# Optimization experiments

Measured on AMD Instinct MI355X. Metric: run time of the kernel, lower is better.

The kernel has to match this reference:

```python
import jax, jax.numpy as jnp
import numpy as np

EPS = 1e-5

def setup_inputs() -> dict:
    key = jax.random.key(0)
    ks = jax.random.split(key, 6)
    N, E, C, H, L = 50000, 800000, 128, 128, 3
    x = jax.random.normal(ks[0], (N, C), dtype=jnp.float32)
    edge_index = jax.random.randint(ks[1], (2, E), 0, N, dtype=jnp.int64)
    # Xavier-ish scaled weights; layer 0 uses in=C=H so all layers stack uniformly.
    Wl = jax.random.normal(ks[2], (L, C, H), dtype=jnp.float32) / np.sqrt(C)
    Wr = jax.random.normal(ks[3], (L, C, H), dtype=jnp.float32) / np.sqrt(C)
    b = jnp.zeros((L, H), dtype=jnp.float32)
    gamma = jnp.ones((L, H), dtype=jnp.float32)
    beta = jnp.zeros((L, H), dtype=jnp.float32)
    return {"x": x, "edge_index": edge_index, "Wl": Wl, "Wr": Wr, "b": b,
            "gamma": gamma, "beta": beta}

def _sage_bn_relu(x, src, dst, Wl, Wr, b, gamma, beta):
    N = x.shape[0]
    # mean aggregation of source features into target nodes (PyG SAGEConv default)
    agg = jax.ops.segment_sum(x[src], dst, num_segments=N)          # [N, C]
    deg = jax.ops.segment_sum(jnp.ones_like(dst, dtype=x.dtype), dst, num_segments=N)
    mean_nbr = agg / jnp.maximum(deg, 1.0)[:, None]
    h = mean_nbr @ Wl + x @ Wr + b                                   # [N, H]
    # BatchNorm1d (training-mode batch statistics over nodes)
    mu = jnp.mean(h, axis=0)
    var = jnp.var(h, axis=0)
    h = gamma * (h - mu) * jax.lax.rsqrt(var + EPS) + beta
    return jax.nn.relu(h)  # dropout omitted (deterministic reference, p->0)

def reference(x, edge_index, Wl, Wr, b, gamma, beta):
    src, dst = edge_index[0], edge_index[1]
    h = x
    for l in range(Wl.shape[0]):
        h = _sage_bn_relu(h, src, dst, Wl[l], Wr[l], b[l], gamma[l], beta[l])
    return h
```

## Files before the change

kernel.cpp:

```cpp
#include <hip/hip_runtime.h>
#include <hip/hip_bf16.h>

#define BN_EPS 1e-5f
#define NPASS 4
#define NKEY 512
#define BCAP2 6144

typedef unsigned short u16;
typedef unsigned int u32;
typedef __attribute__((ext_vector_type(8))) short bf16x8v;
typedef __attribute__((ext_vector_type(4))) float f32x4v;

__device__ __forceinline__ float bf2f(u16 u){
    union { u32 i; float f; } c; c.i = ((u32)u) << 16; return c.f;
}
__device__ __forceinline__ u16 f2bf(float f){
    union { float f; u32 i; } c; c.f = f;
    u32 x = c.i;
    u32 r = x + 0x7FFFu + ((x >> 16) & 1u);
    return (u16)(r >> 16);
}
__device__ __forceinline__ float lo16(u32 u){
    union { u32 i; float f; } c; c.i = u << 16; return c.f;
}
__device__ __forceinline__ float hi16(u32 u){
    union { u32 i; float f; } c; c.i = u & 0xFFFF0000u; return c.f;
}
__device__ __forceinline__ u32 pack2(float f0, float f1){
    return (u32)f2bf(f0) | ((u32)f2bf(f1) << 16);
}

__global__ void detect_k(const int* __restrict__ ei, const u16* __restrict__ xu,
                         int* __restrict__ flags){
    int lane = threadIdx.x;
    unsigned long long bal = __ballot(ei[2 * lane + 1] != 0);
    int cnt = 0;
    #pragma unroll
    for (int k = 0; k < 4; ++k){
        u16 u = xu[2 * (lane + 64 * k)];
        int e = (u >> 7) & 0xFF;
        cnt += (e >= 0x70 && e <= 0x86) ? 1 : 0;
    }
    #pragma unroll
    for (int off = 1; off < 64; off <<= 1) cnt += __shfl_xor(cnt, off);
    if (lane == 0){
        flags[0] = (bal == 0ULL) ? 1 : 0;
        flags[1] = (cnt >= 128) ? 1 : 0;
    }
}

__global__ void prep_k(const void* __restrict__ x, const void* __restrict__ Wl,
                       const void* __restrict__ Wr, const void* __restrict__ b,
                       const void* __restrict__ g, const void* __restrict__ be,
                       u16* __restrict__ xb, u16* __restrict__ wT, float* __restrict__ p,
                       int total4, int wtot, int per, const int* __restrict__ flags){
    int i = blockIdx.x * blockDim.x + threadIdx.x;
    int bf = flags[1];
    if (i < total4){
        if (bf){
            ((uint2*)xb)[i] = ((const uint2*)x)[i];
        } else {
            float4 v = ((const float4*)x)[i];
            ushort4 o; o.x = f2bf(v.x); o.y = f2bf(v.y); o.z = f2bf(v.z); o.w = f2bf(v.w);
            ((ushort4*)xb)[i] = o;
        }
    }
    if (i < wtot){
        u16 vl = bf ? ((const u16*)Wl)[i] : f2bf(((const float*)Wl)[i]);
        u16 vr = bf ? ((const u16*)Wr)[i] : f2bf(((const float*)Wr)[i]);
        int l = i >> 14, r = (i >> 7) & 127, c = i & 127;
        wT[(size_t)(l * 2 + 0) * 16384 + c * 128 + r] = vl;
        wT[(size_t)(l * 2 + 1) * 16384 + c * 128 + r] = vr;
    }
    if (i < per){
        if (bf){
            p[i]           = bf2f(((const u16*)b)[i]);
            p[per + i]     = bf2f(((const u16*)g)[i]);
            p[2 * per + i] = bf2f(((const u16*)be)[i]);
        } else {
            p[i]           = ((const float*)b)[i];
            p[per + i]     = ((const float*)g)[i];
            p[2 * per + i] = ((const float*)be)[i];
        }
    }
}

__global__ __launch_bounds__(1024) void phist_k(const void* __restrict__ ei, int E,
                                                int tile, u32* __restrict__ blockHist,
                                                const int* __restrict__ flags){
    __shared__ u32 lh[NKEY];
    int tid = threadIdx.x;
    if (tid < NKEY) lh[tid] = 0u;
    __syncthreads();
    int start = blockIdx.x * tile;
    int end = min(E, start + tile);
    int i64 = flags[0];
    for (int i = start + tid; i < end; i += 1024){
        int s, d;
        if (i64){
            const long long* p = (const long long*)ei;
            s = (int)p[i]; d = (int)p[E + i];
        } else {
            const int* p = (const int*)ei;
            s = p[i]; d = p[E + i];
        }
        int key = ((s >> 14) << 7) | (d >> 9);
        atomicAdd(&lh[key], 1u);
    }
    __syncthreads();
    if (tid < NKEY) blockHist[blockIdx.x * NKEY + tid] = lh[tid];
}

__global__ __launch_bounds__(512) void bases_k(const u32* __restrict__ blockHist,
                                               u32* __restrict__ blockBase,
                                               int* __restrict__ rangeBase,
                                               int* __restrict__ rp2N, int nb){
    __shared__ u32 t_s[NKEY];
    int k = threadIdx.x;
    u32 run = 0;
    #pragma unroll 8
    for (int b = 0; b < nb; ++b){
        blockBase[b * NKEY + k] = run;
        run += blockHist[b * NKEY + k];
    }
    t_s[k] = min(run, (u32)BCAP2);
    __syncthreads();
    if (k == 0){
        u32 r = 0;
        for (int j = 0; j < NKEY; ++j){ u32 v = t_s[j]; t_s[j] = r; r += v; }
        rangeBase[NKEY] = (int)r;
        *rp2N = (int)r;
    }
    __syncthreads();
    rangeBase[k] = (int)t_s[k];
}

__global__ __launch_bounds__(1024) void pscat_k(const void* __restrict__ ei, int E,
                                                int tile, const u32* __restrict__ blockBase,
                                                u32* __restrict__ part,
                                                const int* __restrict__ flags){
    __shared__ u32 lcur[NKEY];
    int tid = threadIdx.x;
    if (tid < NKEY) lcur[tid] = blockBase[blockIdx.x * NKEY + tid];
    __syncthreads();
    int start = blockIdx.x * tile;
    int end = min(E, start + tile);
    int i64 = flags[0];
    for (int i = start + tid; i < end; i += 1024){
        int s, d;
        if (i64){
            const long long* p = (const long long*)ei;
            s = (int)p[i]; d = (int)p[E + i];
        } else {
            const int* p = (const int*)ei;
            s = p[i]; d = p[E + i];
        }
        int key = ((s >> 14) << 7) | (d >> 9);
        u32 pos = atomicAdd(&lcur[key], 1u);
        if (pos < BCAP2) part[(size_t)key * BCAP2 + pos] = (u32)(u16)s | ((u32)(d & 511) << 16);
    }
}

__global__ __launch_bounds__(1024) void build_k(const u32* __restrict__ part,
                                                const int* __restrict__ rangeBase,
                                                int* __restrict__ rowptr2,
                                                u16* __restrict__ col, int N){
    __shared__ u32 bins[512];
    __shared__ u32 wsum[8];
    __shared__ u16 sorted[BCAP2];
    int key  = blockIdx.x;
    int tid  = threadIdx.x;
    int base = rangeBase[key];
    int cntk = rangeBase[key + 1] - base;
    int p    = key >> 7;
    int d0   = (key & 127) << 9;
    if (tid < 512) bins[tid] = 0u;
    __syncthreads();
    const u32* pk = part + (size_t)key * BCAP2;
    for (int i = tid; i < cntk; i += 1024)
        atomicAdd(&bins[pk[i] >> 16], 1u);
    __syncthreads();
    int lane = tid & 63, w = tid >> 6;
    u32 v = (tid < 512) ? bins[tid] : 0u;
    u32 sc = v;
    #pragma unroll
    for (int off = 1; off < 64; off <<= 1){
        u32 u = __shfl_up(sc, off);
        if (lane >= off) sc += u;
    }
    if (lane == 63 && w < 8) wsum[w] = sc;
    __syncthreads();
    if (tid == 0){
        u32 r = 0;
        #pragma unroll
        for (int j = 0; j < 8; ++j){ u32 t = wsum[j]; wsum[j] = r; r += t; }
    }
    __syncthreads();
    u32 excl = (w < 8 ? wsum[w] : 0u) + sc - v;
    if (tid < 512){
        int d = d0 + tid;
        if (d < N) rowptr2[(size_t)p * N + d] = base + (int)excl;
        bins[tid] = excl;
    }
    __syncthreads();
    for (int i = tid; i < cntk; i += 1024){
        u32 e = pk[i];
        u32 pos = atomicAdd(&bins[e >> 16], 1u);
        sorted[pos] = (u16)e;
    }
    __syncthreads();
    for (int i = tid; i < cntk; i += 1024)
        col[base + i] = sorted[i];
}

#define ACC8(A, G) \
    A[0] += lo16(G.x); A[1] += hi16(G.x); \
    A[2] += lo16(G.y); A[3] += hi16(G.y); \
    A[4] += lo16(G.z); A[5] += hi16(G.z); \
    A[6] += lo16(G.w); A[7] += hi16(G.w);

__global__ __launch_bounds__(256) void agg_k(const u16* __restrict__ h,
                                             const int* __restrict__ rp2,
                                             const u16* __restrict__ col,
                                             u16* __restrict__ meanb, int N){
    int tid  = threadIdx.x;
    int gwid = (blockIdx.x * 256 + tid) >> 6;
    int lane = tid & 63;
    int quad = lane >> 4;
    int sub  = lane & 15;
    if (gwid * 8 >= N) return;
    int d0 = gwid * 8 + quad * 2;
    int d1 = d0 + 1;

    float a0[8] = {0.f,0.f,0.f,0.f,0.f,0.f,0.f,0.f};
    float a1[8] = {0.f,0.f,0.f,0.f,0.f,0.f,0.f,0.f};
    int g0 = 0, g1 = 0;

    for (int p = 0; p < NPASS; ++p){
        const int* rp = rp2 + (size_t)p * N;
        int s0 = 0, e0 = 0, s1 = 0, e1 = 0;
        if (d0 < N){ s0 = rp[d0]; e0 = rp[d0 + 1]; }
        if (d1 < N){ s1 = rp[d1]; e1 = rp[d1 + 1]; }
        g0 += e0 - s0; g1 += e1 - s1;
        int i0 = s0, i1 = s1;
        for (; i0 + 1 < e0 && i1 + 1 < e1; i0 += 2, i1 += 2){
            int sa = col[i0], sb = col[i0 + 1], sc = col[i1], sd = col[i1 + 1];
            uint4 ga = *(const uint4*)(h + (size_t)sa * 128 + sub * 8);
            uint4 gb = *(const uint4*)(h + (size_t)sb * 128 + sub * 8);
            uint4 gc = *(const uint4*)(h + (size_t)sc * 128 + sub * 8);
            uint4 gd = *(const uint4*)(h + (size_t)sd * 128 + sub * 8);
            ACC8(a0, ga); ACC8(a0, gb);
            ACC8(a1, gc); ACC8(a1, gd);
        }
        for (; i0 + 1 < e0; i0 += 2){
            int sa = col[i0], sb = col[i0 + 1];
            uint4 ga = *(const uint4*)(h + (size_t)sa * 128 + sub * 8);
            uint4 gb = *(const uint4*)(h + (size_t)sb * 128 + sub * 8);
            ACC8(a0, ga); ACC8(a0, gb);
        }
        if (i0 < e0){
            int sa = col[i0];
            uint4 ga = *(const uint4*)(h + (size_t)sa * 128 + sub * 8);
            ACC8(a0, ga);
        }
        for (; i1 + 1 < e1; i1 += 2){
            int sc = col[i1], sd = col[i1 + 1];
            uint4 gc = *(const uint4*)(h + (size_t)sc * 128 + sub * 8);
            uint4 gd = *(const uint4*)(h + (size_t)sd * 128 + sub * 8);
            ACC8(a1, gc); ACC8(a1, gd);
        }
        if (i1 < e1){
            int sc = col[i1];
            uint4 gc = *(const uint4*)(h + (size_t)sc * 128 + sub * 8);
            ACC8(a1, gc);
        }
    }

    if (d0 < N){
        float di = 1.f / fmaxf((float)g0, 1.f);
        uint4 o;
        o.x = pack2(a0[0] * di, a0[1] * di);
        o.y = pack2(a0[2] * di, a0[3] * di);
        o.z = pack2(a0[4] * di, a0[5] * di);
        o.w = pack2(a0[6] * di, a0[7] * di);
        *(uint4*)(meanb + (size_t)d0 * 128 + sub * 8) = o;
    }
    if (d1 < N){
        float di = 1.f / fmaxf((float)g1, 1.f);
        uint4 o;
        o.x = pack2(a1[0] * di, a1[1] * di);
        o.y = pack2(a1[2] * di, a1[3] * di);
        o.z = pack2(a1[4] * di, a1[5] * di);
        o.w = pack2(a1[6] * di, a1[7] * di);
        *(uint4*)(meanb + (size_t)d1 * 128 + sub * 8) = o;
    }
}
#undef ACC8

__global__ __launch_bounds__(256, 2) void gemm_k(
        const u16* __restrict__ Aa, const u16* __restrict__ Ab,
        const u16* __restrict__ wT, const float* __restrict__ bias,
        float* __restrict__ stats, u16* __restrict__ hp16, int N, int NT){
    int tid  = threadIdx.x;
    int lane = tid & 63;
    int w    = tid >> 6;
    int hl   = lane & 15;
    int quad = lane >> 4;
    int c0   = (2 * w)     * 16 + hl;
    int c1   = (2 * w + 1) * 16 + hl;

    bf16x8v Bf[2][2][4];
    {
        const u16* bp = wT + (size_t)(2 * w) * 2048 + (size_t)hl * 128 + quad * 8;
        #pragma unroll
        for (int tl = 0; tl < 2; ++tl)
            #pragma unroll
            for (int half = 0; half < 2; ++half)
                #pragma unroll
                for (int kc = 0; kc < 4; ++kc)
                    Bf[tl][half][kc] =
                        *(const bf16x8v*)(bp + tl * 2048 + half * 16384 + kc * 32);
    }
    float bv0 = bias[c0], bv1 = bias[c1];
    float cs0 = 0.f, cq0 = 0.f, cs1 = 0.f, cq1 = 0.f;

    size_t laneoff = (size_t)hl * 128 + quad * 8;
    bf16x8v AX[2][2][4], AY[2][2][4];

#define LOADA(DST, T) { \
    int m0_ = (T) * 32; \
    int rb0_ = m0_;      if (rb0_ + 16 > N) rb0_ = N - 16; \
    int rb1_ = m0_ + 16; if (rb1_ + 16 > N) rb1_ = N - 16; \
    const u16* pa0_ = Aa + (size_t)rb0_ * 128 + laneoff; \
    const u16* pb0_ = Ab + (size_t)rb0_ * 128 + laneoff; \
    const u16* pa1_ = Aa + (size_t)rb1_ * 128 + laneoff; \
    const u16* pb1_ = Ab + (size_t)rb1_ * 128 + laneoff; \
    _Pragma("unroll") \
    for (int kc_ = 0; kc_ < 4; ++kc_){ \
        DST[0][0][kc_] = *(const bf16x8v*)(pa0_ + kc_ * 32); \
        DST[1][0][kc_] = *(const bf16x8v*)(pa1_ + kc_ * 32); \
        DST[0][1][kc_] = *(const bf16x8v*)(pb0_ + kc_ * 32); \
        DST[1][1][kc_] = *(const bf16x8v*)(pb1_ + kc_ * 32); \
    } }

#define PROC(SRC, T) { \
    int m0_ = (T) * 32; \
    int rb0_ = m0_;      bool v0_ = (m0_ + 16 <= N); if (!v0_) rb0_ = N - 16; \
    int rb1_ = m0_ + 16; bool v1_ = (m0_ + 32 <= N); if (!v1_) rb1_ = N - 16; \
    f32x4v acc0_[2], acc1_[2]; \
    acc0_[0] = (f32x4v){0.f,0.f,0.f,0.f}; acc0_[1] = (f32x4v){0.f,0.f,0.f,0.f}; \
    acc1_[0] = (f32x4v){0.f,0.f,0.f,0.f}; acc1_[1] = (f32x4v){0.f,0.f,0.f,0.f}; \
    _Pragma("unroll") \
    for (int half_ = 0; half_ < 2; ++half_) \
        _Pragma("unroll") \
        for (int kc_ = 0; kc_ < 4; ++kc_) \
            _Pragma("unroll") \
            for (int tl_ = 0; tl_ < 2; ++tl_){ \
                acc0_[tl_] = __builtin_amdgcn_mfma_f32_16x16x32_bf16( \
                    SRC[0][half_][kc_], Bf[tl_][half_][kc_], acc0_[tl_], 0, 0, 0); \
                acc1_[tl_] = __builtin_amdgcn_mfma_f32_16x16x32_bf16( \
                    SRC[1][half_][kc_], Bf[tl_][half_][kc_], acc1_[tl_], 0, 0, 0); \
            } \
    _Pragma("unroll") \
    for (int tl_ = 0; tl_ < 2; ++tl_){ \
        int   c_  = tl_ ? c1 : c0; \
        float bv_ = tl_ ? bv1 : bv0; \
        if (v0_){ \
            _Pragma("unroll") \
            for (int r_ = 0; r_ < 4; ++r_){ \
                float vv_ = acc0_[tl_][r_] + bv_; \
                hp16[(size_t)(rb0_ + quad * 4 + r_) * 128 + c_] = f2bf(vv_); \
                if (tl_){ cs1 += vv_; cq1 += vv_ * vv_; } else { cs0 += vv_; cq0 += vv_ * vv_; } \
            } \
        } \
        if (v1_){ \
            _Pragma("unroll") \
            for (int r_ = 0; r_ < 4; ++r_){ \
                float vv_ = acc1_[tl_][r_] + bv_; \
                hp16[(size_t)(rb1_ + quad * 4 + r_) * 128 + c_] = f2bf(vv_); \
                if (tl_){ cs1 += vv_; cq1 += vv_ * vv_; } else { cs0 += vv_; cq0 += vv_ * vv_; } \
            } \
        } \
    } }

    int t = blockIdx.x;
    int G = gridDim.x;
    if (t < NT){
        LOADA(AX, t);
        for (;;){
            int tn = t + G;
            if (tn < NT) LOADA(AY, tn);
            PROC(AX, t);
            t = tn;
            if (t >= NT) break;
            tn = t + G;
            if (tn < NT) LOADA(AX, tn);
            PROC(AY, t);
            t = tn;
            if (t >= NT) break;
        }
    }
#undef LOADA
#undef PROC

    cs0 += __shfl_xor(cs0, 16); cs0 += __shfl_xor(cs0, 32);
    cq0 += __shfl_xor(cq0, 16); cq0 += __shfl_xor(cq0, 32);
    cs1 += __shfl_xor(cs1, 16); cs1 += __shfl_xor(cs1, 32);
    cq1 += __shfl_xor(cq1, 16); cq1 += __shfl_xor(cq1, 32);
    if (quad == 0){
        float* st = stats + (size_t)(blockIdx.x & 63) * 256;
        atomicAdd(&st[c0],       cs0);
        atomicAdd(&st[128 + c0], cq0);
        atomicAdd(&st[c1],       cs1);
        atomicAdd(&st[128 + c1], cq1);
    }
}

__global__ __launch_bounds__(256) void apply_k(
        const u16* __restrict__ in, const float* __restrict__ stats,
        const float* __restrict__ g, const float* __restrict__ be,
        u16* __restrict__ outb, float* __restrict__ outf, int use_f32,
        int total4, float invN){
    __shared__ float s_red[256];
    __shared__ float s_ss[256];
    int tid = threadIdx.x;
    float s = 0.f;
    #pragma unroll 8
    for (int bkt = 0; bkt < 64; ++bkt) s += stats[bkt * 256 + tid];
    s_red[tid] = s;
    __syncthreads();
    if (tid < 128){
        float mu  = s_red[tid] * invN;
        float var = s_red[128 + tid] * invN - mu * mu;
        if (!(mu == mu)) mu = 0.f;
        if (!(var >= 0.f) || !(var == var)) var = 0.f;
        float sc = g[tid] * rsqrtf(var + BN_EPS);
        s_ss[tid]       = sc;
        s_ss[128 + tid] = be[tid] - mu * sc;
    }
    __syncthreads();
    int c = (tid & 31) * 4;
    float sc0 = s_ss[c],     sh0 = s_ss[128 + c];
    float sc1 = s_ss[c + 1], sh1 = s_ss[129 + c];
    float sc2 = s_ss[c + 2], sh2 = s_ss[130 + c];
    float sc3 = s_ss[c + 3], sh3 = s_ss[131 + c];
    for (int i = blockIdx.x * blockDim.x + tid; i < total4; i += blockDim.x * gridDim.x){
        uint2 u = ((const uint2*)in)[i];
        float4 v;
        v.x = lo16(u.x); v.y = hi16(u.x); v.z = lo16(u.y); v.w = hi16(u.y);
        if (!(v.x == v.x)) v.x = 0.f;
        if (!(v.y == v.y)) v.y = 0.f;
        if (!(v.z == v.z)) v.z = 0.f;
        if (!(v.w == v.w)) v.w = 0.f;
        float r0 = fmaxf(v.x * sc0 + sh0, 0.f);
        float r1 = fmaxf(v.y * sc1 + sh1, 0.f);
        float r2 = fmaxf(v.z * sc2 + sh2, 0.f);
        float r3 = fmaxf(v.w * sc3 + sh3, 0.f);
        if (use_f32){
            float4 o; o.x = r0; o.y = r1; o.z = r2; o.w = r3;
            ((float4*)outf)[i] = o;
        } else {
            uint2 o; o.x = pack2(r0, r1); o.y = pack2(r2, r3);
            ((uint2*)outb)[i] = o;
        }
    }
}

extern "C" void kernel_launch(void* const* d_in, const int* in_sizes, int n_in,
                              void* d_out, int out_size, void* d_ws, size_t ws_size,
                              hipStream_t stream){
    const void* x  = d_in[0];
    const int*  ei = (const int*)d_in[1];
    const void* Wl = d_in[2];
    const void* Wr = d_in[3];
    const void* b  = d_in[4];
    const void* gm = d_in[5];
    const void* bt = d_in[6];
    float* outf = (float*)d_out;

    const int N = in_sizes[0] / 128;
    const int E = in_sizes[1] / 2;
    const int L = in_sizes[2] / 16384;
    const int PB = 128;
    const int TILE = (E + PB - 1) / PB;

    char* wsp = (char*)d_ws;
    size_t off = 0;
    auto alloc = [&](size_t bytes) -> char* {
        char* p = wsp + off;
        off = (off + bytes + 255) & ~(size_t)255;
        return p;
    };
    int*   flags  = (int*)  alloc(16);
    int*   rowptr2= (int*)  alloc(((size_t)NPASS * N + 1) * 4);
    u16*   col    = (u16*)  alloc((size_t)E * 2);
    u32*   bHist  = (u32*)  alloc((size_t)PB * NKEY * 4);
    u32*   bBase  = (u32*)  alloc((size_t)PB * NKEY * 4);
    int*   rangeB = (int*)  alloc((size_t)(NKEY + 1) * 4);
    u32*   part   = (u32*)  alloc((size_t)NKEY * BCAP2 * 4);
    u16*   wT     = (u16*)  alloc((size_t)L * 2 * 16384 * 2);
    float* pvec   = (float*)alloc((size_t)3 * L * 128 * 4);
    float* stats  = (float*)alloc((size_t)L * 64 * 256 * 4);
    u16*   xb     = (u16*)  alloc((size_t)N * 128 * 2);
    u16*   meanb  = (u16*)  alloc((size_t)N * 128 * 2);
    u16*   hpre16 = (u16*)  alloc((size_t)N * 128 * 2);
    u16*   hA     = (u16*)  alloc((size_t)N * 128 * 2);
    u16*   hB     = (u16*)  alloc((size_t)N * 128 * 2);
    (void)ws_size; (void)n_in; (void)out_size;

    detect_k<<<1, 64, 0, stream>>>(ei, (const u16*)x, flags);
    hipMemsetAsync(stats, 0, (size_t)L * 64 * 256 * 4, stream);

    phist_k<<<PB, 1024, 0, stream>>>((const void*)ei, E, TILE, bHist, flags);
    bases_k<<<1, 512, 0, stream>>>(bHist, bBase, rangeB, rowptr2 + (size_t)NPASS * N, PB);
    pscat_k<<<PB, 1024, 0, stream>>>((const void*)ei, E, TILE, bBase, part, flags);
    build_k<<<NKEY, 1024, 0, stream>>>(part, rangeB, rowptr2, col, N);

    prep_k<<<(N * 32 + 255) / 256, 256, 0, stream>>>(x, Wl, Wr, b, gm, bt, xb, wT, pvec,
                                                     N * 32, L * 16384, L * 128, flags);

    const u16* state = xb;
    int NT      = (N + 31) / 32;
    int gblocks = (NT + 2) / 3;
    int nwaves  = (N + 7) / 8;
    int ablocks = (nwaves + 3) / 4;
    float invN  = 1.f / (float)N;
    for (int l = 0; l < L; ++l){
        int last = (l == L - 1);
        u16* nxt = (l & 1) ? hB : hA;
        agg_k<<<ablocks, 256, 0, stream>>>(state, rowptr2, col, meanb, N);
        gemm_k<<<gblocks, 256, 0, stream>>>(meanb, state, wT + (size_t)l * 2 * 16384,
                                            pvec + (size_t)l * 128,
                                            stats + (size_t)l * 64 * 256,
                                            hpre16, N, NT);
        apply_k<<<1024, 256, 0, stream>>>(hpre16, stats + (size_t)l * 64 * 256,
                                          pvec + (size_t)L * 128 + l * 128,
                                          pvec + (size_t)2 * L * 128 + l * 128,
                                          nxt, outf, last, N * 32, invN);
        state = nxt;
    }
}
```

Baseline: 320.1 us.

## Stage GEMM A tiles through swizzled double-buffered LDS shared by all waves

Previously each of the four waves loaded the full 32-row A tile (mean and self features) from global memory into registers, so every tile was read four times. Now each wave loads a quarter of the tile into registers, writes it to a double-buffered, XOR-swizzled LDS buffer, and all waves read their MFMA fragments from LDS. This cuts redundant global and L2 traffic and register pressure, at the cost of 32KB of LDS per block and a __syncthreads per tile. The removed `if (t < NT)` guard assumes the grid never exceeds the tile count.

Result: faster. 283.1 us (median of 2 runs) (-11.6%).

```diff
diff --git a/kernel.cpp b/kernel.cpp
--- a/kernel.cpp
+++ b/kernel.cpp
@@ -301,6 +301,7 @@
         const u16* __restrict__ Aa, const u16* __restrict__ Ab,
         const u16* __restrict__ wT, const float* __restrict__ bias,
         float* __restrict__ stats, u16* __restrict__ hp16, int N, int NT){
+    __shared__ __align__(16) u16 sA[16384];
     int tid  = threadIdx.x;
     int lane = tid & 63;
     int w    = tid >> 6;
@@ -324,29 +325,54 @@
     float bv0 = bias[c0], bv1 = bias[c1];
     float cs0 = 0.f, cq0 = 0.f, cs1 = 0.f, cq1 = 0.f;
 
-    size_t laneoff = (size_t)hl * 128 + quad * 8;
-    bf16x8v AX[2][2][4], AY[2][2][4];
-
-#define LOADA(DST, T) { \
+    int smat[4], srow[4], ssub[4], sldo[4];
+    #pragma unroll
+    for (int i = 0; i < 4; ++i){
+        int kk  = w * 4 + i;
+        int off = (kk & 7) * 1024 + lane * 16;
+        int mat = kk >> 3;
+        int row = off >> 8;
+        int sub = (off >> 4) & 15;
+        smat[i] = mat; srow[i] = row; ssub[i] = sub;
+        sldo[i] = mat * 4096 + row * 128 + ((sub ^ (row & 7)) * 8);
+    }
+    uint4 rg0, rg1, rg2, rg3;
+
+#define STAGE_REGS(T) { \
     int m0_ = (T) * 32; \
     int rb0_ = m0_;      if (rb0_ + 16 > N) rb0_ = N - 16; \
     int rb1_ = m0_ + 16; if (rb1_ + 16 > N) rb1_ = N - 16; \
-    const u16* pa0_ = Aa + (size_t)rb0_ * 128 + laneoff; \
-    const u16* pb0_ = Ab + (size_t)rb0_ * 128 + laneoff; \
-    const u16* pa1_ = Aa + (size_t)rb1_ * 128 + laneoff; \
-    const u16* pb1_ = Ab + (size_t)rb1_ * 128 + laneoff; \
     _Pragma("unroll") \
-    for (int kc_ = 0; kc_ < 4; ++kc_){ \
-        DST[0][0][kc_] = *(const bf16x8v*)(pa0_ + kc_ * 32); \
-        DST[1][0][kc_] = *(const bf16x8v*)(pa1_ + kc_ * 32); \
-        DST[0][1][kc_] = *(const bf16x8v*)(pb0_ + kc_ * 32); \
-        DST[1][1][kc_] = *(const bf16x8v*)(pb1_ + kc_ * 32); \
+    for (int i_ = 0; i_ < 4; ++i_){ \
+        int row_  = srow[i_]; \
+        int grow_ = (row_ < 16) ? (rb0_ + row_) : (rb1_ + row_ - 16); \
+        const u16* src_ = (smat[i_] ? Ab : Aa) + (size_t)grow_ * 128 + ssub[i_] * 8; \
+        uint4 v_ = *(const uint4*)src_; \
+        if (i_ == 0) rg0 = v_; else if (i_ == 1) rg1 = v_; \
+        else if (i_ == 2) rg2 = v_; else rg3 = v_; \
     } }
 
-#define PROC(SRC, T) { \
+#define STAGE_WRITE(B) { \
+    u16* bb_ = sA + (B) * 8192; \
+    *(uint4*)(bb_ + sldo[0]) = rg0; \
+    *(uint4*)(bb_ + sldo[1]) = rg1; \
+    *(uint4*)(bb_ + sldo[2]) = rg2; \
+    *(uint4*)(bb_ + sldo[3]) = rg3; }
+
+#define COMPUTE(B, T) { \
     int m0_ = (T) * 32; \
     int rb0_ = m0_;      bool v0_ = (m0_ + 16 <= N); if (!v0_) rb0_ = N - 16; \
     int rb1_ = m0_ + 16; bool v1_ = (m0_ + 32 <= N); if (!v1_) rb1_ = N - 16; \
+    const u16* base_ = sA + (B) * 8192; \
+    bf16x8v Af[2][2][4];    \
+    _Pragma("unroll") \
+    for (int kc_ = 0; kc_ < 4; ++kc_){ \
+        int sl_ = ((quad + kc_ * 4) ^ (hl & 7)) * 8; \
+        Af[0][0][kc_] = *(const bf16x8v*)(base_ +        hl * 128        + sl_); \
+        Af[1][0][kc_] = *(const bf16x8v*)(base_ + (16 + hl) * 128        + sl_); \
+        Af[0][1][kc_] = *(const bf16x8v*)(base_ + 4096 +        hl * 128 + sl_); \
+        Af[1][1][kc_] = *(const bf16x8v*)(base_ + 4096 + (16 + hl) * 128 + sl_); \
+    } \
     f32x4v acc0_[2], acc1_[2]; \
     acc0_[0] = (f32x4v){0.f,0.f,0.f,0.f}; acc0_[1] = (f32x4v){0.f,0.f,0.f,0.f}; \
     acc1_[0] = (f32x4v){0.f,0.f,0.f,0.f}; acc1_[1] = (f32x4v){0.f,0.f,0.f,0.f}; \
@@ -357,9 +383,9 @@
             _Pragma("unroll") \
             for (int tl_ = 0; tl_ < 2; ++tl_){ \
                 acc0_[tl_] = __builtin_amdgcn_mfma_f32_16x16x32_bf16( \
-                    SRC[0][half_][kc_], Bf[tl_][half_][kc_], acc0_[tl_], 0, 0, 0); \
+                    Af[0][half_][kc_], Bf[tl_][half_][kc_], acc0_[tl_], 0, 0, 0); \
                 acc1_[tl_] = __builtin_amdgcn_mfma_f32_16x16x32_bf16( \
-                    SRC[1][half_][kc_], Bf[tl_][half_][kc_], acc1_[tl_], 0, 0, 0); \
+                    Af[1][half_][kc_], Bf[tl_][half_][kc_], acc1_[tl_], 0, 0, 0); \
             } \
     _Pragma("unroll") \
     for (int tl_ = 0; tl_ < 2; ++tl_){ \
@@ -385,23 +411,24 @@
 
     int t = blockIdx.x;
     int G = gridDim.x;
-    if (t < NT){
-        LOADA(AX, t);
-        for (;;){
-            int tn = t + G;
-            if (tn < NT) LOADA(AY, tn);
-            PROC(AX, t);
-            t = tn;
-            if (t >= NT) break;
-            tn = t + G;
-            if (tn < NT) LOADA(AX, tn);
-            PROC(AY, t);
-            t = tn;
-            if (t >= NT) break;
-        }
-    }
-#undef LOADA
-#undef PROC
+    int cur = 0;
+    STAGE_REGS(t);
+    STAGE_WRITE(0);
+    __syncthreads();
+    for (;;){
+        int tn = t + G;
+        bool hN = (tn < NT);
+        if (hN) STAGE_REGS(tn);
+        COMPUTE(cur, t);
+        if (!hN) break;
+        STAGE_WRITE(cur ^ 1);
+        __syncthreads();
+        cur ^= 1;
+        t = tn;
+    }
+#undef STAGE_REGS
+#undef STAGE_WRITE
+#undef COMPUTE
 
     cs0 += __shfl_xor(cs0, 16); cs0 += __shfl_xor(cs0, 32);
     cq0 += __shfl_xor(cq0, 16); cq0 += __shfl_xor(cq0, 32);
```
